# Performance work log

Measured on AMD Instinct MI355X. Metric: run time of the kernel, lower is better.

## Reference

```python
import jax, jax.numpy as jnp
import numpy as np

B, N, MAX_T, NUM_CLASSES = 128, 1024, 64, 80
PRED_DIM = 5 + NUM_CLASSES  # 85; cls logits are pred[:, 6:] per the source (79 classes)


def setup_inputs() -> dict:
    key = jax.random.key(0)
    k1, k2, k3 = jax.random.split(key, 3)
    preds = jax.random.normal(k1, (B, N, PRED_DIM), dtype=jnp.float32)
    # well-formed boxes: two random corners per target, sorted so x1<=x2, y1<=y2
    corners = jax.random.uniform(k2, (B, MAX_T, 2, 2), dtype=jnp.float32)
    lo = jnp.min(corners, axis=2)
    hi = jnp.max(corners, axis=2)
    # class id in [-1, 78]; -1 marks an invalid (padded) target
    cls_id = jax.random.randint(k3, (B, MAX_T), -1, NUM_CLASSES - 1).astype(jnp.float32)
    targets = jnp.concatenate([lo, hi, cls_id[..., None]], axis=-1)  # (B, MAX_T, 5)
    return {"preds": preds, "targets": targets}


def _pairwise_iou(pb, tb):
    # pb: (N,4), tb: (M,4) -> (N,M)
    x1 = jnp.maximum(pb[:, None, 0], tb[None, :, 0])
    y1 = jnp.maximum(pb[:, None, 1], tb[None, :, 1])
    x2 = jnp.minimum(pb[:, None, 2], tb[None, :, 2])
    y2 = jnp.minimum(pb[:, None, 3], tb[None, :, 3])
    inter = jnp.clip(x2 - x1, 0.0) * jnp.clip(y2 - y1, 0.0)
    a1 = (pb[:, 2] - pb[:, 0]) * (pb[:, 3] - pb[:, 1])
    a2 = (tb[:, 2] - tb[:, 0]) * (tb[:, 3] - tb[:, 1])
    union = a1[:, None] + a2[None, :] - inter
    return inter / (union + 1e-6)


def _loss_one(pred, tgt):
    n = pred.shape[0]
    valid = tgt[:, 4] >= 0.0                      # (M,)
    kv = valid.sum()
    ious = _pairwise_iou(pred[:, :4], tgt[:, :4])  # (N,M)
    ious = jnp.where(valid[None, :], ious, -1.0)   # invalid targets never match
    best_ious = ious.max(axis=1)                   # (N,)
    best_idx = ious.argmax(axis=1)                 # (N,)
    matched_raw = best_ious > 0.5
    matched = jnp.where(matched_raw.any(), matched_raw, best_ious == best_ious.max())
    m = matched.astype(pred.dtype)
    u = 1.0 - m
    mcnt = m.sum()
    ucnt = u.sum()

    mt = tgt[best_idx]                             # (N,5) matched targets
    # SmoothL1 (beta=1), masked mean over matched rows x 4 coords
    d = pred[:, :4] - mt[:, :4]
    ad = jnp.abs(d)
    sl1 = jnp.where(ad < 1.0, 0.5 * d * d, ad - 0.5)
    bbox_loss = (sl1 * m[:, None]).sum() / jnp.maximum(mcnt * 4.0, 1.0)

    # cross entropy over pred[:, 6:] (faithful to source slicing)
    logits = pred[:, 6:]
    labels = jnp.clip(mt[:, 4].astype(jnp.int32), 0, logits.shape[1] - 1)
    ce = jax.nn.logsumexp(logits, axis=-1) - jnp.take_along_axis(logits, labels[:, None], axis=1)[:, 0]
    cls_loss = (ce * m).sum() / jnp.maximum(mcnt, 1.0)

    conf_logit = pred[:, 4]
    conf_m = (jax.nn.softplus(-conf_logit) * m).sum() / jnp.maximum(mcnt, 1.0)  # BCE vs 1
    conf_u = (jax.nn.softplus(conf_logit) * u).sum() / jnp.maximum(ucnt, 1.0)   # BCE vs 0
    conf_loss = jnp.where(ucnt > 0, (conf_m + conf_u) * 0.5, conf_m)

    loss_valid = bbox_loss + cls_loss + conf_loss
    loss_novalid = jax.nn.softplus(conf_logit).mean()  # BCE vs all-zero targets
    return jnp.where(kv > 0, loss_valid, loss_novalid)


def reference(preds, targets):
    per_sample = jax.vmap(_loss_one)(preds, targets)  # (B,)
    return per_sample.sum() / preds.shape[0]
```

## Files before the change

kernel.cpp:

```cpp
#include <hip/hip_runtime.h>
#include <math.h>

#define NPRED 1024
#define NT 64
#define PD 85
#define NLOGIT 79
#define ROWS 256
#define QBLK 4

__device__ __forceinline__ float softplusf(float x) {
    return fmaxf(x, 0.0f) + log1pf(expf(-fabsf(x)));
}


__global__ __launch_bounds__(256)
void k1_match(const float* __restrict__ preds,
              const float* __restrict__ targets,
              float* __restrict__ part, int nblk)
{
    const int bx  = blockIdx.x;
    const int b   = bx >> 2;
    const int q   = bx & 3;
    const int tid = threadIdx.x;
    const int r   = q * ROWS + tid;

    __shared__ float tgs[NT * 5];
    __shared__ float tx1[NT], ty1[NT], tx2[NT], ty2[NT], tcl[NT], ta[NT];
    __shared__ int   tv[NT];
    __shared__ float red[4][11];
    __shared__ float redm[4];
    __shared__ float bmax_s;
    __shared__ int   kv_s;

    const float* pp = preds + ((size_t)b * NPRED + r) * PD;
    const float px1 = pp[0], py1 = pp[1], px2 = pp[2], py2 = pp[3], conf = pp[4];

    if (tid < (NT * 5 / 4))
        ((float4*)tgs)[tid] = ((const float4*)(targets + (size_t)b * NT * 5))[tid];
    __syncthreads();
    if (tid < NT) {
        float a = tgs[tid*5], c = tgs[tid*5+1], d = tgs[tid*5+2], e = tgs[tid*5+3], f = tgs[tid*5+4];
        tx1[tid]=a; ty1[tid]=c; tx2[tid]=d; ty2[tid]=e; tcl[tid]=f;
        ta[tid] = (d - a) * (e - c);
        tv[tid] = (f >= 0.0f) ? 1 : 0;
        unsigned long long bl = __ballot(f >= 0.0f);
        if (tid == 0) kv_s = (int)__popcll(bl);
    }
    __syncthreads();

    const float parea = (px2 - px1) * (py2 - py1);
    float best = -INFINITY;
    int   bidx = 0;
    #pragma unroll 8
    for (int t = 0; t < NT; ++t) {
        float w = fminf(px2, tx2[t]) - fmaxf(px1, tx1[t]); w = fmaxf(w, 0.0f);
        float h = fminf(py2, ty2[t]) - fmaxf(py1, ty1[t]); h = fmaxf(h, 0.0f);
        float inter = w * h;
        float uni   = parea + ta[t] - inter;
        float iou   = tv[t] ? inter / (uni + 1e-6f) : -1.0f;
        if (iou > best) { best = iou; bidx = t; }
    }

    {
        float v = best;
        #pragma unroll
        for (int o = 32; o > 0; o >>= 1) v = fmaxf(v, __shfl_down(v, o));
        if ((tid & 63) == 0) redm[tid >> 6] = v;
        __syncthreads();
        if (tid == 0) bmax_s = fmaxf(fmaxf(redm[0], redm[1]), fmaxf(redm[2], redm[3]));
        __syncthreads();
    }
    const float bmax = bmax_s;
    const bool cA = (best > 0.5f);
    const bool cB = (best == bmax);

    const float sp = softplusf(conf);
    float vals[11];
    #pragma unroll
    for (int j = 0; j < 11; ++j) vals[j] = 0.0f;
    vals[0] = sp;

    if (cA || cB) {
        float d0 = px1 - tx1[bidx], d1 = py1 - ty1[bidx];
        float d2 = px2 - tx2[bidx], d3 = py2 - ty2[bidx];
        float bb = 0.0f;
        {
            float dd[4] = { d0, d1, d2, d3 };
            #pragma unroll
            for (int i = 0; i < 4; ++i) {
                float ad = fabsf(dd[i]);
                bb += (ad < 1.0f) ? 0.5f * dd[i] * dd[i] : ad - 0.5f;
            }
        }
        const float* lg = pp + 6;
        float m = -INFINITY, s = 0.0f;
        #pragma unroll
        for (int i = 0; i < NLOGIT; ++i) {
            float v  = lg[i];
            float nm = fmaxf(m, v);
            s = s * expf(m - nm) + expf(v - nm);
            m = nm;
        }
        const float lse = m + logf(s);
        int label = (int)tcl[bidx];
        label = label < 0 ? 0 : (label > NLOGIT - 1 ? NLOGIT - 1 : label);
        const float cev = lse - pp[6 + label];
        const float sfm = softplusf(-conf);

        if (cA) { vals[1] += 1.0f; vals[2] += bb; vals[3] += cev; vals[4] += sfm; vals[5] += sp; }
        if (cB) { vals[6] += 1.0f; vals[7] += bb; vals[8] += cev; vals[9] += sfm; vals[10] += sp; }
    }

    #pragma unroll
    for (int j = 0; j < 11; ++j) {
        float v = vals[j];
        #pragma unroll
        for (int o = 32; o > 0; o >>= 1) v += __shfl_down(v, o);
        if ((tid & 63) == 0) red[tid >> 6][j] = v;
    }
    __syncthreads();
    if (tid < 11)  part[(size_t)tid * nblk + bx] = red[0][tid] + red[1][tid] + red[2][tid] + red[3][tid];
    if (tid == 11) part[(size_t)11  * nblk + bx] = bmax;
    if (tid == 12) part[(size_t)12  * nblk + bx] = (float)kv_s;
}

__global__ __launch_bounds__(512)
void k2_final(const float* __restrict__ part, float* __restrict__ out,
              int nb, int nblk)
{
    const int t = threadIdx.x;
    const int s = t >> 2, k = t & 3;
    const int bx = s * 4 + k;

    __shared__ float ps[128];
    __shared__ float r2[2];

    float v[13];
    #pragma unroll
    for (int j = 0; j < 13; ++j) v[j] = part[(size_t)j * nblk + bx];

    float pmax_k = v[11];
    float gmax = pmax_k;
    gmax = fmaxf(gmax, __shfl_xor(gmax, 1));
    gmax = fmaxf(gmax, __shfl_xor(gmax, 2));
    const float mB = (pmax_k == gmax) ? 1.0f : 0.0f;
    v[6] *= mB; v[7] *= mB; v[8] *= mB; v[9] *= mB; v[10] *= mB;
    #pragma unroll
    for (int j = 0; j < 11; ++j) {
        v[j] += __shfl_xor(v[j], 1);
        v[j] += __shfl_xor(v[j], 2);
    }

    if (k == 0) {
        const float sp_total = v[0];
        const bool  anym = (v[1] > 0.0f);
        const float mcnt = anym ? v[1] : v[6];
        const float bboxs = anym ? v[2] : v[7];
        const float ces   = anym ? v[3] : v[8];
        const float sfms  = anym ? v[4] : v[9];
        const float spms  = anym ? v[5] : v[10];
        const float ucnt = (float)NPRED - mcnt;
        const float sfus = sp_total - spms;
        const float bbox_loss = bboxs / fmaxf(mcnt * 4.0f, 1.0f);
        const float cls_loss  = ces   / fmaxf(mcnt, 1.0f);
        const float conf_m    = sfms  / fmaxf(mcnt, 1.0f);
        const float conf_u    = sfus  / fmaxf(ucnt, 1.0f);
        const float conf_loss = (ucnt > 0.0f) ? (conf_m + conf_u) * 0.5f : conf_m;
        const float loss_valid   = bbox_loss + cls_loss + conf_loss;
        const float loss_novalid = sp_total / (float)NPRED;
        const int   kv = (int)v[12];
        ps[s] = (kv > 0) ? loss_valid : loss_novalid;
    }
    __syncthreads();

    if (t < 128) {
        float x = (t < nb) ? ps[t] : 0.0f;
        #pragma unroll
        for (int o = 32; o > 0; o >>= 1) x += __shfl_down(x, o);
        if ((t & 63) == 0) r2[t >> 6] = x;
    }
    __syncthreads();
    if (t == 0) out[0] = (r2[0] + r2[1]) / (float)nb;
}

extern "C" void kernel_launch(void* const* d_in, const int* in_sizes, int n_in,
                              void* d_out, int out_size, void* d_ws, size_t ws_size,
                              hipStream_t stream) {
    const float* preds   = (const float*)d_in[0];
    const float* targets = (const float*)d_in[1];
    float* out  = (float*)d_out;
    float* part = (float*)d_ws;

    const int nb   = in_sizes[0] / (NPRED * PD);
    const int nblk = nb * QBLK;

    hipLaunchKernelGGL(k1_match, dim3(nblk), dim3(ROWS), 0, stream,
                       preds, targets, part, nblk);
    hipLaunchKernelGGL(k2_final, dim3(1), dim3(nb * 4), 0, stream,
                       part, out, nb, nblk);
}
```

Measured before the change: 30.53 us.

## Fuse match and final reduction into one cooperative kernel with grid sync

Merges the two-kernel pipeline into a single cooperative launch in which all 512 blocks write partials, synchronize with a grid-wide barrier, and block 0 then does the per-sample combine and the final mean. Target boxes in shared memory are also packed into float4/float2 arrays so each loop iteration reads them with fewer LDS loads. The aim is to remove the second kernel launch and its gap. In exchange it adds cooperative-launch overhead and a grid barrier across 512 blocks, and the final stage runs serially in one block.

```diff
diff --git a/kernel.cpp b/kernel.cpp
--- a/kernel.cpp
+++ b/kernel.cpp
@@ -1,5 +1,8 @@
 #include <hip/hip_runtime.h>
+#include <hip/hip_cooperative_groups.h>
 #include <math.h>
+
+namespace cg = cooperative_groups;
 
 #define NPRED 1024
 #define NT 64
@@ -7,6 +10,7 @@
 #define NLOGIT 79
 #define ROWS 256
 #define QBLK 4
+#define NB 128
 
 __device__ __forceinline__ float softplusf(float x) {
     return fmaxf(x, 0.0f) + log1pf(expf(-fabsf(x)));
@@ -14,9 +18,11 @@
 
 
 __global__ __launch_bounds__(256)
-void k1_match(const float* __restrict__ preds,
-              const float* __restrict__ targets,
-              float* __restrict__ part, int nblk)
+void fused_detloss(const float* __restrict__ preds,
+                   const float* __restrict__ targets,
+                   float* __restrict__ part,
+                   float* __restrict__ out,
+                   int nb, int nblk)
 {
     const int bx  = blockIdx.x;
     const int b   = bx >> 2;
@@ -24,13 +30,16 @@
     const int tid = threadIdx.x;
     const int r   = q * ROWS + tid;
 
-    __shared__ float tgs[NT * 5];
-    __shared__ float tx1[NT], ty1[NT], tx2[NT], ty2[NT], tcl[NT], ta[NT];
-    __shared__ int   tv[NT];
-    __shared__ float red[4][11];
-    __shared__ float redm[4];
-    __shared__ float bmax_s;
-    __shared__ int   kv_s;
+    __shared__ float  tgs[NT * 5];
+    __shared__ float4 tb[NT];
+    __shared__ float2 tav[NT];
+    __shared__ float  tcl[NT];
+    __shared__ float  red[4][11];
+    __shared__ float  redm[4];
+    __shared__ float  bmax_s;
+    __shared__ int    kv_s;
+    __shared__ float  ps[NB];
+    __shared__ float  r2[2];
 
     const float* pp = preds + ((size_t)b * NPRED + r) * PD;
     const float px1 = pp[0], py1 = pp[1], px2 = pp[2], py2 = pp[3], conf = pp[4];
@@ -40,9 +49,9 @@
     __syncthreads();
     if (tid < NT) {
         float a = tgs[tid*5], c = tgs[tid*5+1], d = tgs[tid*5+2], e = tgs[tid*5+3], f = tgs[tid*5+4];
-        tx1[tid]=a; ty1[tid]=c; tx2[tid]=d; ty2[tid]=e; tcl[tid]=f;
-        ta[tid] = (d - a) * (e - c);
-        tv[tid] = (f >= 0.0f) ? 1 : 0;
+        tb[tid]  = make_float4(a, c, d, e);
+        tav[tid] = make_float2((d - a) * (e - c), (f >= 0.0f) ? 1.0f : 0.0f);
+        tcl[tid] = f;
         unsigned long long bl = __ballot(f >= 0.0f);
         if (tid == 0) kv_s = (int)__popcll(bl);
     }
@@ -53,11 +62,13 @@
     int   bidx = 0;
     #pragma unroll 8
     for (int t = 0; t < NT; ++t) {
-        float w = fminf(px2, tx2[t]) - fmaxf(px1, tx1[t]); w = fmaxf(w, 0.0f);
-        float h = fminf(py2, ty2[t]) - fmaxf(py1, ty1[t]); h = fmaxf(h, 0.0f);
+        const float4 tt = tb[t];
+        const float2 av = tav[t];
+        float w = fminf(px2, tt.z) - fmaxf(px1, tt.x); w = fmaxf(w, 0.0f);
+        float h = fminf(py2, tt.w) - fmaxf(py1, tt.y); h = fmaxf(h, 0.0f);
         float inter = w * h;
-        float uni   = parea + ta[t] - inter;
-        float iou   = tv[t] ? inter / (uni + 1e-6f) : -1.0f;
+        float uni   = parea + av.x - inter;
+        float iou   = (av.y != 0.0f) ? inter / (uni + 1e-6f) : -1.0f;
         if (iou > best) { best = iou; bidx = t; }
     }
 
@@ -81,16 +92,13 @@
     vals[0] = sp;
 
     if (cA || cB) {
-        float d0 = px1 - tx1[bidx], d1 = py1 - ty1[bidx];
-        float d2 = px2 - tx2[bidx], d3 = py2 - ty2[bidx];
+        const float4 mt = tb[bidx];
+        float dd[4] = { px1 - mt.x, py1 - mt.y, px2 - mt.z, py2 - mt.w };
         float bb = 0.0f;
-        {
-            float dd[4] = { d0, d1, d2, d3 };
-            #pragma unroll
-            for (int i = 0; i < 4; ++i) {
-                float ad = fabsf(dd[i]);
-                bb += (ad < 1.0f) ? 0.5f * dd[i] * dd[i] : ad - 0.5f;
-            }
+        #pragma unroll
+        for (int i = 0; i < 4; ++i) {
+            float ad = fabsf(dd[i]);
+            bb += (ad < 1.0f) ? 0.5f * dd[i] * dd[i] : ad - 0.5f;
         }
         const float* lg = pp + 6;
         float m = -INFINITY, s = 0.0f;
@@ -122,65 +130,61 @@
     if (tid < 11)  part[(size_t)tid * nblk + bx] = red[0][tid] + red[1][tid] + red[2][tid] + red[3][tid];
     if (tid == 11) part[(size_t)11  * nblk + bx] = bmax;
     if (tid == 12) part[(size_t)12  * nblk + bx] = (float)kv_s;
-}
-
-__global__ __launch_bounds__(512)
-void k2_final(const float* __restrict__ part, float* __restrict__ out,
-              int nb, int nblk)
-{
-    const int t = threadIdx.x;
-    const int s = t >> 2, k = t & 3;
-    const int bx = s * 4 + k;
-
-    __shared__ float ps[128];
-    __shared__ float r2[2];
-
-    float v[13];
-    #pragma unroll
-    for (int j = 0; j < 13; ++j) v[j] = part[(size_t)j * nblk + bx];
-
-    float pmax_k = v[11];
-    float gmax = pmax_k;
-    gmax = fmaxf(gmax, __shfl_xor(gmax, 1));
-    gmax = fmaxf(gmax, __shfl_xor(gmax, 2));
-    const float mB = (pmax_k == gmax) ? 1.0f : 0.0f;
-    v[6] *= mB; v[7] *= mB; v[8] *= mB; v[9] *= mB; v[10] *= mB;
-    #pragma unroll
-    for (int j = 0; j < 11; ++j) {
-        v[j] += __shfl_xor(v[j], 1);
-        v[j] += __shfl_xor(v[j], 2);
-    }
-
-    if (k == 0) {
-        const float sp_total = v[0];
-        const bool  anym = (v[1] > 0.0f);
-        const float mcnt = anym ? v[1] : v[6];
-        const float bboxs = anym ? v[2] : v[7];
-        const float ces   = anym ? v[3] : v[8];
-        const float sfms  = anym ? v[4] : v[9];
-        const float spms  = anym ? v[5] : v[10];
-        const float ucnt = (float)NPRED - mcnt;
-        const float sfus = sp_total - spms;
-        const float bbox_loss = bboxs / fmaxf(mcnt * 4.0f, 1.0f);
-        const float cls_loss  = ces   / fmaxf(mcnt, 1.0f);
-        const float conf_m    = sfms  / fmaxf(mcnt, 1.0f);
-        const float conf_u    = sfus  / fmaxf(ucnt, 1.0f);
-        const float conf_loss = (ucnt > 0.0f) ? (conf_m + conf_u) * 0.5f : conf_m;
-        const float loss_valid   = bbox_loss + cls_loss + conf_loss;
-        const float loss_novalid = sp_total / (float)NPRED;
-        const int   kv = (int)v[12];
-        ps[s] = (kv > 0) ? loss_valid : loss_novalid;
-    }
-    __syncthreads();
-
-    if (t < 128) {
-        float x = (t < nb) ? ps[t] : 0.0f;
-        #pragma unroll
-        for (int o = 32; o > 0; o >>= 1) x += __shfl_down(x, o);
-        if ((t & 63) == 0) r2[t >> 6] = x;
-    }
-    __syncthreads();
-    if (t == 0) out[0] = (r2[0] + r2[1]) / (float)nb;
+
+    cg::this_grid().sync();
+
+    if (bx == 0) {
+        if (tid < nb) {
+            const int s0 = tid * QBLK;
+            float bm[QBLK];
+            #pragma unroll
+            for (int i = 0; i < QBLK; ++i) bm[i] = part[(size_t)11 * nblk + s0 + i];
+            float gmax = bm[0];
+            #pragma unroll
+            for (int i = 1; i < QBLK; ++i) gmax = fmaxf(gmax, bm[i]);
+
+            float sp_total = 0.0f;
+            float A[5] = {0,0,0,0,0};
+            float Bv[5] = {0,0,0,0,0};
+            #pragma unroll
+            for (int i = 0; i < QBLK; ++i) {
+                const int idx = s0 + i;
+                sp_total += part[(size_t)0 * nblk + idx];
+                #pragma unroll
+                for (int j = 0; j < 5; ++j) A[j] += part[(size_t)(1 + j) * nblk + idx];
+                const float mB = (bm[i] == gmax) ? 1.0f : 0.0f;
+                #pragma unroll
+                for (int j = 0; j < 5; ++j) Bv[j] += mB * part[(size_t)(6 + j) * nblk + idx];
+            }
+            const int kv = (int)part[(size_t)12 * nblk + s0];
+
+            const bool  anym = (A[0] > 0.0f);
+            const float mcnt = anym ? A[0] : Bv[0];
+            const float bboxs= anym ? A[1] : Bv[1];
+            const float ces  = anym ? A[2] : Bv[2];
+            const float sfms = anym ? A[3] : Bv[3];
+            const float spms = anym ? A[4] : Bv[4];
+            const float ucnt = (float)NPRED - mcnt;
+            const float sfus = sp_total - spms;
+            const float bbox_loss = bboxs / fmaxf(mcnt * 4.0f, 1.0f);
+            const float cls_loss  = ces   / fmaxf(mcnt, 1.0f);
+            const float conf_m    = sfms  / fmaxf(mcnt, 1.0f);
+            const float conf_u    = sfus  / fmaxf(ucnt, 1.0f);
+            const float conf_loss = (ucnt > 0.0f) ? (conf_m + conf_u) * 0.5f : conf_m;
+            const float loss_valid   = bbox_loss + cls_loss + conf_loss;
+            const float loss_novalid = sp_total / (float)NPRED;
+            ps[tid] = (kv > 0) ? loss_valid : loss_novalid;
+        }
+        __syncthreads();
+        if (tid < NB) {
+            float x = (tid < nb) ? ps[tid] : 0.0f;
+            #pragma unroll
+            for (int o = 32; o > 0; o >>= 1) x += __shfl_down(x, o);
+            if ((tid & 63) == 0) r2[tid >> 6] = x;
+        }
+        __syncthreads();
+        if (tid == 0) out[0] = (r2[0] + r2[1]) / (float)nb;
+    }
 }
 
 extern "C" void kernel_launch(void* const* d_in, const int* in_sizes, int n_in,
@@ -191,11 +195,11 @@
     float* out  = (float*)d_out;
     float* part = (float*)d_ws;
 
-    const int nb   = in_sizes[0] / (NPRED * PD);
-    const int nblk = nb * QBLK;
-
-    hipLaunchKernelGGL(k1_match, dim3(nblk), dim3(ROWS), 0, stream,
-                       preds, targets, part, nblk);
-    hipLaunchKernelGGL(k2_final, dim3(1), dim3(nb * 4), 0, stream,
-                       part, out, nb, nblk);
+    int nb   = in_sizes[0] / (NPRED * PD);
+    int nblk = nb * QBLK;
+
+    void* args[] = { (void*)&preds, (void*)&targets, (void*)&part,
+                     (void*)&out, (void*)&nb, (void*)&nblk };
+    hipLaunchCooperativeKernel((void*)fused_detloss, dim3(nblk), dim3(ROWS),
+                               args, 0, stream);
 }
```

After: 77.69 us. 2.54x slower.

## Split each prediction row across two threads for IoU matching and logsumexp

Applied to the files above, without the earlier changes.

Each prediction row is now handled by a pair of threads: each half scans 32 of the 64 targets and half of the logits, and the pair merges its argmax and online-softmax state through lane shuffles. The grid doubles to 8 blocks per sample with 128 rows each, and target data is packed into float4/float2 shared arrays to cut the number of LDS reads. The final reduction kernel is widened to 8 partials per sample with 1024 threads. The aim is more parallelism and shorter serial per-thread loops, at the cost of extra shuffles and of redundant loads of the box fields in both threads of a pair.

```diff
diff --git a/kernel.cpp b/kernel.cpp
--- a/kernel.cpp
+++ b/kernel.cpp
@@ -5,32 +5,36 @@
 #define NT 64
 #define PD 85
 #define NLOGIT 79
-#define ROWS 256
-#define QBLK 4
+#define QBLK 8
+#define RPB 128
+#define THREADS 256
 
 __device__ __forceinline__ float softplusf(float x) {
     return fmaxf(x, 0.0f) + log1pf(expf(-fabsf(x)));
 }
 
 
-__global__ __launch_bounds__(256)
+__global__ __launch_bounds__(THREADS)
 void k1_match(const float* __restrict__ preds,
               const float* __restrict__ targets,
               float* __restrict__ part, int nblk)
 {
-    const int bx  = blockIdx.x;
-    const int b   = bx >> 2;
-    const int q   = bx & 3;
-    const int tid = threadIdx.x;
-    const int r   = q * ROWS + tid;
-
-    __shared__ float tgs[NT * 5];
-    __shared__ float tx1[NT], ty1[NT], tx2[NT], ty2[NT], tcl[NT], ta[NT];
-    __shared__ int   tv[NT];
-    __shared__ float red[4][11];
-    __shared__ float redm[4];
-    __shared__ float bmax_s;
-    __shared__ int   kv_s;
+    const int bx   = blockIdx.x;
+    const int b    = bx >> 3;
+    const int q    = bx & 7;
+    const int tid  = threadIdx.x;
+    const int row  = tid >> 1;
+    const int half = tid & 1;
+    const int r    = q * RPB + row;
+
+    __shared__ float  tgs[NT * 5];
+    __shared__ float4 tb[NT];
+    __shared__ float2 tav[NT];
+    __shared__ float  tcl[NT];
+    __shared__ float  red[4][11];
+    __shared__ float  redm[4];
+    __shared__ float  bmax_s;
+    __shared__ int    kv_s;
 
     const float* pp = preds + ((size_t)b * NPRED + r) * PD;
     const float px1 = pp[0], py1 = pp[1], px2 = pp[2], py2 = pp[3], conf = pp[4];
@@ -40,29 +44,42 @@
     __syncthreads();
     if (tid < NT) {
         float a = tgs[tid*5], c = tgs[tid*5+1], d = tgs[tid*5+2], e = tgs[tid*5+3], f = tgs[tid*5+4];
-        tx1[tid]=a; ty1[tid]=c; tx2[tid]=d; ty2[tid]=e; tcl[tid]=f;
-        ta[tid] = (d - a) * (e - c);
-        tv[tid] = (f >= 0.0f) ? 1 : 0;
+        tb[tid]  = make_float4(a, c, d, e);
+        tav[tid] = make_float2((d - a) * (e - c), (f >= 0.0f) ? 1.0f : 0.0f);
+        tcl[tid] = f;
         unsigned long long bl = __ballot(f >= 0.0f);
         if (tid == 0) kv_s = (int)__popcll(bl);
     }
     __syncthreads();
 
     const float parea = (px2 - px1) * (py2 - py1);
+    const int t0 = half * 32;
     float best = -INFINITY;
-    int   bidx = 0;
+    int   bidx = t0;
     #pragma unroll 8
-    for (int t = 0; t < NT; ++t) {
-        float w = fminf(px2, tx2[t]) - fmaxf(px1, tx1[t]); w = fmaxf(w, 0.0f);
-        float h = fminf(py2, ty2[t]) - fmaxf(py1, ty1[t]); h = fmaxf(h, 0.0f);
+    for (int i = 0; i < 32; ++i) {
+        const int t = t0 + i;
+        const float4 tt = tb[t];
+        const float2 av = tav[t];
+        float w = fminf(px2, tt.z) - fmaxf(px1, tt.x); w = fmaxf(w, 0.0f);
+        float h = fminf(py2, tt.w) - fmaxf(py1, tt.y); h = fmaxf(h, 0.0f);
         float inter = w * h;
-        float uni   = parea + ta[t] - inter;
-        float iou   = tv[t] ? inter / (uni + 1e-6f) : -1.0f;
+        float uni   = parea + av.x - inter;
+        float iou   = (av.y != 0.0f) ? inter / (uni + 1e-6f) : -1.0f;
         if (iou > best) { best = iou; bidx = t; }
     }
 
+    const float obest = __shfl_xor(best, 1);
+    const int   obidx = __shfl_xor(bidx, 1);
+    const float bA = half ? obest : best;
+    const int   iA = half ? obidx : bidx;
+    const float bB = half ? best  : obest;
+    const int   iB = half ? bidx  : obidx;
+    const float fbest = (bA >= bB) ? bA : bB;
+    const int   fidx  = (bA >= bB) ? iA : iB;
+
     {
-        float v = best;
+        float v = fbest;
         #pragma unroll
         for (int o = 32; o > 0; o >>= 1) v = fmaxf(v, __shfl_down(v, o));
         if ((tid & 63) == 0) redm[tid >> 6] = v;
@@ -71,44 +88,50 @@
         __syncthreads();
     }
     const float bmax = bmax_s;
-    const bool cA = (best > 0.5f);
-    const bool cB = (best == bmax);
+    const bool cA = (fbest > 0.5f);
+    const bool cB = (fbest == bmax);
 
     const float sp = softplusf(conf);
     float vals[11];
     #pragma unroll
     for (int j = 0; j < 11; ++j) vals[j] = 0.0f;
-    vals[0] = sp;
+    if (half == 0) vals[0] = sp;
 
     if (cA || cB) {
-        float d0 = px1 - tx1[bidx], d1 = py1 - ty1[bidx];
-        float d2 = px2 - tx2[bidx], d3 = py2 - ty2[bidx];
-        float bb = 0.0f;
-        {
-            float dd[4] = { d0, d1, d2, d3 };
+        const float* lg = pp + 6;
+        const int base = half * 40;
+        const int len  = half ? 39 : 40;
+        float m = -INFINITY, s = 0.0f;
+        #pragma unroll 8
+        for (int i = 0; i < len; ++i) {
+            float v  = lg[base + i];
+            float nm = fmaxf(m, v);
+            s = s * expf(m - nm) + expf(v - nm);
+            m = nm;
+        }
+        const float om = __shfl_xor(m, 1);
+        const float os = __shfl_xor(s, 1);
+        const float nm = fmaxf(m, om);
+        const float st = s * expf(m - nm) + os * expf(om - nm);
+        const float lse = nm + logf(st);
+
+        if (half == 0) {
+            const float4 mt = tb[fidx];
+            float dd[4] = { px1 - mt.x, py1 - mt.y, px2 - mt.z, py2 - mt.w };
+            float bb = 0.0f;
             #pragma unroll
             for (int i = 0; i < 4; ++i) {
                 float ad = fabsf(dd[i]);
                 bb += (ad < 1.0f) ? 0.5f * dd[i] * dd[i] : ad - 0.5f;
             }
+            int label = (int)tcl[fidx];
+            label = label < 0 ? 0 : (label > NLOGIT - 1 ? NLOGIT - 1 : label);
+            const float cev = lse - lg[label];
+            const float sfm = softplusf(-conf);
+
+            if (cA) { vals[1] += 1.0f; vals[2] += bb; vals[3] += cev; vals[4] += sfm; vals[5] += sp; }
+            if (cB) { vals[6] += 1.0f; vals[7] += bb; vals[8] += cev; vals[9] += sfm; vals[10] += sp; }
         }
-        const float* lg = pp + 6;
-        float m = -INFINITY, s = 0.0f;
-        #pragma unroll
-        for (int i = 0; i < NLOGIT; ++i) {
-            float v  = lg[i];
-            float nm = fmaxf(m, v);
-            s = s * expf(m - nm) + expf(v - nm);
-            m = nm;
-        }
-        const float lse = m + logf(s);
-        int label = (int)tcl[bidx];
-        label = label < 0 ? 0 : (label > NLOGIT - 1 ? NLOGIT - 1 : label);
-        const float cev = lse - pp[6 + label];
-        const float sfm = softplusf(-conf);
-
-        if (cA) { vals[1] += 1.0f; vals[2] += bb; vals[3] += cev; vals[4] += sfm; vals[5] += sp; }
-        if (cB) { vals[6] += 1.0f; vals[7] += bb; vals[8] += cev; vals[9] += sfm; vals[10] += sp; }
     }
 
     #pragma unroll
@@ -124,13 +147,13 @@
     if (tid == 12) part[(size_t)12  * nblk + bx] = (float)kv_s;
 }
 
-__global__ __launch_bounds__(512)
+__global__ __launch_bounds__(1024)
 void k2_final(const float* __restrict__ part, float* __restrict__ out,
               int nb, int nblk)
 {
     const int t = threadIdx.x;
-    const int s = t >> 2, k = t & 3;
-    const int bx = s * 4 + k;
+    const int s = t >> 3, k = t & 7;
+    const int bx = s * 8 + k;
 
     __shared__ float ps[128];
     __shared__ float r2[2];
@@ -139,26 +162,26 @@
     #pragma unroll
     for (int j = 0; j < 13; ++j) v[j] = part[(size_t)j * nblk + bx];
 
-    float pmax_k = v[11];
-    float gmax = pmax_k;
-    gmax = fmaxf(gmax, __shfl_xor(gmax, 1));
-    gmax = fmaxf(gmax, __shfl_xor(gmax, 2));
-    const float mB = (pmax_k == gmax) ? 1.0f : 0.0f;
-    v[6] *= mB; v[7] *= mB; v[8] *= mB; v[9] *= mB; v[10] *= mB;
+    float gmax = v[11];
+    #pragma unroll
+    for (int o = 1; o < 8; o <<= 1) gmax = fmaxf(gmax, __shfl_xor(gmax, o));
+    const float mB = (v[11] == gmax) ? 1.0f : 0.0f;
+    #pragma unroll
+    for (int j = 6; j <= 10; ++j) v[j] *= mB;
     #pragma unroll
     for (int j = 0; j < 11; ++j) {
-        v[j] += __shfl_xor(v[j], 1);
-        v[j] += __shfl_xor(v[j], 2);
-    }
-
-    if (k == 0) {
+        #pragma unroll
+        for (int o = 1; o < 8; o <<= 1) v[j] += __shfl_xor(v[j], o);
+    }
+
+    if (k == 0 && s < nb) {
         const float sp_total = v[0];
         const bool  anym = (v[1] > 0.0f);
         const float mcnt = anym ? v[1] : v[6];
-        const float bboxs = anym ? v[2] : v[7];
-        const float ces   = anym ? v[3] : v[8];
-        const float sfms  = anym ? v[4] : v[9];
-        const float spms  = anym ? v[5] : v[10];
+        const float bboxs= anym ? v[2] : v[7];
+        const float ces  = anym ? v[3] : v[8];
+        const float sfms = anym ? v[4] : v[9];
+        const float spms = anym ? v[5] : v[10];
         const float ucnt = (float)NPRED - mcnt;
         const float sfus = sp_total - spms;
         const float bbox_loss = bboxs / fmaxf(mcnt * 4.0f, 1.0f);
@@ -194,8 +217,8 @@
     const int nb   = in_sizes[0] / (NPRED * PD);
     const int nblk = nb * QBLK;
 
-    hipLaunchKernelGGL(k1_match, dim3(nblk), dim3(ROWS), 0, stream,
+    hipLaunchKernelGGL(k1_match, dim3(nblk), dim3(THREADS), 0, stream,
                        preds, targets, part, nblk);
-    hipLaunchKernelGGL(k2_final, dim3(1), dim3(nb * 4), 0, stream,
+    hipLaunchKernelGGL(k2_final, dim3(1), dim3(1024), 0, stream,
                        part, out, nb, nblk);
 }
```

After: 30.63 us. No clear change (+0.3%).
